# Kernel tuning notes

Hardware: AMD Instinct MI355X
Metric: run time of the kernel (lower is better)

## Reference

```python
import jax, jax.numpy as jnp
import numpy as np
from jax import lax

N = 100000   # n_nodes
E = 600000   # n_edges (no self loops by construction)
D = 128      # hidden_dim
L = 3        # n_hops
K = 5        # tail_k_threshold


def setup_inputs() -> dict:
    key = jax.random.key(0)
    ks = jax.random.split(key, 10)
    x = jax.random.normal(ks[0], (N, D), dtype=jnp.float32)
    src = jax.random.randint(ks[1], (E,), 0, N)
    off = jax.random.randint(ks[2], (E,), 1, N)
    dst = (src + off) % N  # guarantees dst != src (self loops removed in original)
    s = 1.0 / np.sqrt(D)
    def U(k, shape):
        return jax.random.uniform(k, shape, minval=-s, maxval=s, dtype=jnp.float32)
    return {
        "x": x,
        "G1": U(ks[3], (L, D, D)), "G2": U(ks[4], (L, D, D)),
        "B1": U(ks[5], (L, D, D)), "B2": U(ks[6], (L, D, D)),
        "R": U(ks[7], (L, D)),
        "edge_src": src, "edge_dst": dst,
    }


def _lrelu(v):
    return jax.nn.leaky_relu(v, 0.2)


def reference(x, G1, G2, B1, B2, R, edge_src, edge_dst):
    # row degrees of adj (A[src, dst] = 1)
    deg = jax.ops.segment_sum(jnp.ones(E, jnp.float32), edge_src, num_segments=N)
    inv_d = jnp.where(deg > 0, 1.0 / jnp.maximum(deg, 1.0), 0.0)   # left norm D^-1 A
    inv_d1 = 1.0 / (deg + 1.0)                                      # (A+I) left norm
    inv_d2 = 1.0 / (deg + 2.0)                                      # +1 virtual node
    w0, w1, w2 = inv_d[edge_src], inv_d1[edge_src], inv_d2[edge_src]
    head_mask = deg > K

    def spmm(w_edge, h):  # (D^-1 A) @ h via gather-scale-scatter
        return jax.ops.segment_sum(w_edge[:, None] * h[edge_dst], edge_src, num_segments=N)

    def propagate(head):
        h = x
        embs = [h]
        sups = []
        for l in range(L):
            nb = spmm(w0, h)
            ft = lax.stop_gradient(h)
            nbd = lax.stop_gradient(nb)
            gamma = _lrelu(ft @ G1[l].T + nbd @ G2[l].T) + 1.0
            beta = _lrelu(ft @ B1[l].T + nbd @ B2[l].T)
            m = ft + gamma * R[l] + beta - nbd   # missing_info (Relation, ablation=0)
            sups.append(m)
            if head:
                h = spmm(w1, h) + inv_d1[:, None] * h
            else:
                h = spmm(w2, h) + inv_d2[:, None] * h + m * inv_d2[:, None]
            embs.append(h)
        emb = jnp.mean(jnp.stack(embs, 0), 0)
        sup = jnp.mean(jnp.stack(sups, 0), 0)
        return emb, sup

    emb_h, _ = propagate(True)
    emb_t, _ = propagate(False)
    node_emb = jnp.where(head_mask[:, None], emb_h, emb_t)
    return node_emb
```

## Files before the change

### kernel.cpp

```cpp
#include <hip/hip_runtime.h>

#define N_NODES 100000
#define N_EDGES 600000
#define DIM 128
#define SCAN_B 1024
#define NCHUNK 98

typedef __attribute__((ext_vector_type(4))) float f32x4;
typedef __attribute__((ext_vector_type(8))) short bf16x8;
typedef __attribute__((ext_vector_type(4))) unsigned short u16x4;
typedef __attribute__((ext_vector_type(8))) unsigned short u16x8;

__device__ __forceinline__ unsigned short f2bf(float f) {
    union { float f; unsigned u; } cv; cv.f = f;
    unsigned r = (cv.u + 0x7FFFu + ((cv.u >> 16) & 1u)) >> 16;
    return (unsigned short)r;
}
__device__ __forceinline__ float bf2f(unsigned short v) {
    union { unsigned u; float f; } c; c.u = ((unsigned)v) << 16; return c.f;
}


__global__ void k_degree(const int* __restrict__ src, int* __restrict__ degi) {
    int e = blockIdx.x * 256 + threadIdx.x;
    if (e < N_EDGES) atomicAdd(&degi[src[e]], 1);
}

__global__ void k_chunksum(const int* __restrict__ degi, int* __restrict__ bsum) {
    __shared__ int sm[SCAN_B];
    int i = blockIdx.x * SCAN_B + threadIdx.x;
    sm[threadIdx.x] = (i < N_NODES) ? degi[i] : 0;
    __syncthreads();
    for (int s = SCAN_B / 2; s > 0; s >>= 1) {
        if (threadIdx.x < (unsigned)s) sm[threadIdx.x] += sm[threadIdx.x + s];
        __syncthreads();
    }
    if (threadIdx.x == 0) bsum[blockIdx.x] = sm[0];
}

__global__ void k_scanb(int* __restrict__ bsum, int nb) {
    __shared__ int sm[128];
    int t = threadIdx.x;
    int v = (t < nb) ? bsum[t] : 0;
    sm[t] = v; __syncthreads();
    for (int s = 1; s < 128; s <<= 1) {
        int a = (t >= s) ? sm[t - s] : 0;
        __syncthreads();
        sm[t] += a;
        __syncthreads();
    }
    if (t < nb) bsum[t] = sm[t] - v;
}

__global__ void k_rowptr(const int* __restrict__ degi, const int* __restrict__ bsum,
                         int* __restrict__ rowptr, int* __restrict__ cnt,
                         float* __restrict__ inv0, float* __restrict__ inv1,
                         float* __restrict__ inv2) {
    __shared__ int sm[SCAN_B];
    int i = blockIdx.x * SCAN_B + threadIdx.x;
    int v = (i < N_NODES) ? degi[i] : 0;
    sm[threadIdx.x] = v; __syncthreads();
    for (int s = 1; s < SCAN_B; s <<= 1) {
        int a = (threadIdx.x >= (unsigned)s) ? sm[threadIdx.x - s] : 0;
        __syncthreads();
        sm[threadIdx.x] += a;
        __syncthreads();
    }
    if (i < N_NODES) {
        int excl = bsum[blockIdx.x] + sm[threadIdx.x] - v;
        rowptr[i] = excl;
        cnt[i] = excl;
        float d = (float)v;
        inv0[i] = (v > 0) ? 1.0f / d : 0.0f;
        inv1[i] = 1.0f / (d + 1.0f);
        inv2[i] = 1.0f / (d + 2.0f);
    }
}

__global__ void k_fill(const int* __restrict__ src, const int* __restrict__ dst,
                       int* __restrict__ cnt, int* __restrict__ col) {
    int e = blockIdx.x * 256 + threadIdx.x;
    if (e < N_EDGES) {
        int pos = atomicAdd(&cnt[src[e]], 1);
        col[pos] = dst[e];
    }
}

__global__ void k_pack(const float* __restrict__ G1, const float* __restrict__ G2,
                       const float* __restrict__ B1, const float* __restrict__ B2,
                       short* __restrict__ Wp) {
    int idx = blockIdx.x * 256 + threadIdx.x;
    int j = idx & 7, lane = (idx >> 3) & 63, nt = (idx >> 9) & 15, kb = (idx >> 13) & 7, l = idx >> 16;
    int k = kb * 32 + (lane >> 4) * 8 + j;
    int n = nt * 16 + (lane & 15);
    float v;
    if (n < 128) {
        v = (k < 128) ? G1[(l * 128 + n) * 128 + k] : G2[(l * 128 + n) * 128 + (k - 128)];
    } else {
        int n2 = n - 128;
        v = (k < 128) ? B1[(l * 128 + n2) * 128 + k] : B2[(l * 128 + n2) * 128 + (k - 128)];
    }
    Wp[idx] = (short)f2bf(v);
}

__global__ void k_xcast(const float* __restrict__ x, unsigned short* __restrict__ xb) {
    int i = (blockIdx.x * 256 + threadIdx.x) * 4;
    f32x4 v = *(const f32x4*)(x + i);
    unsigned short o0 = f2bf(v[0]), o1 = f2bf(v[1]), o2 = f2bf(v[2]), o3 = f2bf(v[3]);
    unsigned long long pk = (unsigned long long)o0 | ((unsigned long long)o1 << 16)
                          | ((unsigned long long)o2 << 32) | ((unsigned long long)o3 << 48);
    *(unsigned long long*)(xb + i) = pk;
}


__device__ __forceinline__ void gather4(const u16x8* __restrict__ h8,
        const int* __restrict__ col, int start, int d, int lane, float* acc) {
    int c = lane & 15;
    int base = lane & 48;
    int dd = d < 16 ? d : 16;
    int idx = (c < dd) ? col[start + c] : 0;
    int dm = d;
    int tmx = __shfl_xor(dm, 16);
    dm = dm > tmx ? dm : tmx;
    tmx = __shfl_xor(dm, 32);
    dm = dm > tmx ? dm : tmx;
    int dmain = dm < 16 ? dm : 16;
    int e = 0;
    for (; e + 2 <= dmain; e += 2) {
        int c0 = __shfl(idx, base + e, 64);
        int c1 = __shfl(idx, base + e + 1, 64);
        if (e < d) {
            u16x8 v = h8[(size_t)c0 * 16 + c];
#pragma unroll
            for (int j = 0; j < 8; ++j) acc[j] += bf2f(v[j]);
        }
        if (e + 1 < d) {
            u16x8 v = h8[(size_t)c1 * 16 + c];
#pragma unroll
            for (int j = 0; j < 8; ++j) acc[j] += bf2f(v[j]);
        }
    }
    if (e < dmain) {
        int c0 = __shfl(idx, base + e, 64);
        if (e < d) {
            u16x8 v = h8[(size_t)c0 * 16 + c];
#pragma unroll
            for (int j = 0; j < 8; ++j) acc[j] += bf2f(v[j]);
        }
        ++e;
    }
    if (dm > 16) {
        for (; e < d; ++e) {
            int c0 = col[start + e];
            u16x8 v = h8[(size_t)c0 * 16 + c];
#pragma unroll
            for (int j = 0; j < 8; ++j) acc[j] += bf2f(v[j]);
        }
    }
}

__global__ __launch_bounds__(256) void k_agg_head4(
    const unsigned short* __restrict__ hsrc, unsigned short* __restrict__ hnext,
    const unsigned short* __restrict__ xb, const unsigned short* __restrict__ h1b,
    float* __restrict__ outp, const float* __restrict__ inv1,
    const int* __restrict__ rowptr, const int* __restrict__ degi,
    const int* __restrict__ col, int final_hop)
{
    int lane = threadIdx.x & 63;
    int wid = (blockIdx.x * 256 + threadIdx.x) >> 6;
    int g = lane >> 4, c = lane & 15;
    int row = wid * 4 + g;
    int start = rowptr[row], d = degi[row];
    float acc[8] = {0,0,0,0,0,0,0,0};
    gather4((const u16x8*)hsrc, col, start, d, lane, acc);
    u16x8 hv = ((const u16x8*)hsrc)[(size_t)row * 16 + c];
    float w = inv1[row];
    float hn[8];
#pragma unroll
    for (int j = 0; j < 8; ++j) hn[j] = w * (acc[j] + bf2f(hv[j]));
    if (!final_hop) {
        u16x8 ho;
#pragma unroll
        for (int j = 0; j < 8; ++j) ho[j] = f2bf(hn[j]);
        ((u16x8*)hnext)[(size_t)row * 16 + c] = ho;
    } else {
        u16x8 xv = ((const u16x8*)xb)[(size_t)row * 16 + c];
        u16x8 h1 = ((const u16x8*)h1b)[(size_t)row * 16 + c];
        f32x4 e0, e1;
#pragma unroll
        for (int j = 0; j < 4; ++j)
            e0[j] = 0.25f * (bf2f(xv[j]) + bf2f(h1[j]) + bf2f(hv[j]) + hn[j]);
#pragma unroll
        for (int j = 0; j < 4; ++j)
            e1[j] = 0.25f * (bf2f(xv[4 + j]) + bf2f(h1[4 + j]) + bf2f(hv[4 + j]) + hn[4 + j]);
        float* op = outp + (size_t)row * DIM + c * 8;
        *(f32x4*)op = e0;
        *(f32x4*)(op + 4) = e1;
    }
}

__global__ __launch_bounds__(256) void k_tail_fused(
    const unsigned short* __restrict__ hb,
    unsigned short* __restrict__ hA, int write_hA,
    unsigned short* __restrict__ hb_next,
    const unsigned short* __restrict__ xb, const unsigned short* __restrict__ h1b,
    float* __restrict__ outp,
    const float* __restrict__ Rl, const short* __restrict__ Wp,
    const float* __restrict__ inv0, const float* __restrict__ inv1,
    const float* __restrict__ inv2,
    const int* __restrict__ rowptr, const int* __restrict__ degi,
    const int* __restrict__ col, int last)
{
    __shared__ __align__(16) unsigned short sS[16][136];

    int wave = threadIdx.x >> 6, lane = threadIdx.x & 63;
    int rb = blockIdx.x * 16;

    {
        int g = lane >> 4, c = lane & 15;
        int row = rb + wave * 4 + g;
        int start = rowptr[row], d = degi[row];
        float acc[8] = {0,0,0,0,0,0,0,0};
        gather4((const u16x8*)hb, col, start, d, lane, acc);
        u16x8 so;
#pragma unroll
        for (int j = 0; j < 8; ++j) so[j] = f2bf(acc[j]);
        *(u16x8*)&sS[wave * 4 + g][c * 8] = so;
        if (write_hA) {
            u16x8 xv = ((const u16x8*)hb)[(size_t)row * 16 + c];
            float w1 = inv1[row];
            u16x8 ho;
#pragma unroll
            for (int j = 0; j < 8; ++j) ho[j] = f2bf(w1 * (acc[j] + bf2f(xv[j])));
            ((u16x8*)hA)[(size_t)row * 16 + c] = ho;
        }
    }
    __syncthreads();

    int q = lane >> 4, m = lane & 15;
    int rowA = rb + m;
    float w0 = inv0[rowA];
    const unsigned short* hrow = hb + (size_t)rowA * DIM + q * 8;
    const short* wl = Wp + lane * 8;

    const f32x4 vz = {0.f, 0.f, 0.f, 0.f};
    f32x4 aA[2] = {vz, vz}, aB[2] = {vz, vz};

#pragma unroll
    for (int kb = 0; kb < 4; ++kb) {
        bf16x8 ah = *(const bf16x8*)(hrow + kb * 32);
#pragma unroll
        for (int j = 0; j < 2; ++j) {
            bf16x8 b1v = *(const bf16x8*)(wl + (kb * 16 + 2 * wave + j) * 512);
            bf16x8 b2v = *(const bf16x8*)(wl + (kb * 16 + 2 * wave + 8 + j) * 512);
            aA[j] = __builtin_amdgcn_mfma_f32_16x16x32_bf16(ah, b1v, aA[j], 0, 0, 0);
            aB[j] = __builtin_amdgcn_mfma_f32_16x16x32_bf16(ah, b2v, aB[j], 0, 0, 0);
        }
    }
#pragma unroll
    for (int kb = 0; kb < 4; ++kb) {
        u16x8 sv = *(const u16x8*)&sS[m][kb * 32 + q * 8];
        bf16x8 as;
#pragma unroll
        for (int j = 0; j < 8; ++j) as[j] = (short)f2bf(w0 * bf2f(sv[j]));
#pragma unroll
        for (int j = 0; j < 2; ++j) {
            bf16x8 b1v = *(const bf16x8*)(wl + ((kb + 4) * 16 + 2 * wave + j) * 512);
            bf16x8 b2v = *(const bf16x8*)(wl + ((kb + 4) * 16 + 2 * wave + 8 + j) * 512);
            aA[j] = __builtin_amdgcn_mfma_f32_16x16x32_bf16(as, b1v, aA[j], 0, 0, 0);
            aB[j] = __builtin_amdgcn_mfma_f32_16x16x32_bf16(as, b2v, aB[j], 0, 0, 0);
        }
    }

    float Rv[2];
#pragma unroll
    for (int j = 0; j < 2; ++j) Rv[j] = Rl[(2 * wave + j) * 16 + m];

#pragma unroll
    for (int r = 0; r < 4; ++r) {
        int gi = rb + q * 4 + r;
        float wi0 = inv0[gi], wi2 = inv2[gi];
        int dgi = degi[gi];
#pragma unroll
        for (int j = 0; j < 2; ++j) {
            int cc = (2 * wave + j) * 16 + m;
            float z1 = aA[j][r], z2 = aB[j][r];
            float h = bf2f(hb[(size_t)gi * DIM + cc]);
            float sva = bf2f(sS[q * 4 + r][cc]);
            float ga = (z1 > 0.f ? z1 : 0.2f * z1) + 1.0f;
            float be = (z2 > 0.f ? z2 : 0.2f * z2);
            float mm = h + ga * Rv[j] + be - wi0 * sva;
            float hn = wi2 * (sva + h + mm);
            if (!last) {
                hb_next[(size_t)gi * DIM + cc] = f2bf(hn);
            } else if (dgi <= 5) {
                float xv = bf2f(xb[(size_t)gi * DIM + cc]);
                float t1 = bf2f(h1b[(size_t)gi * DIM + cc]);
                outp[(size_t)gi * DIM + cc] = 0.25f * (xv + t1 + h + hn);
            }
        }
    }
}


extern "C" void kernel_launch(void* const* d_in, const int* in_sizes, int n_in,
                              void* d_out, int out_size, void* d_ws, size_t ws_size,
                              hipStream_t stream) {
    const float* x  = (const float*)d_in[0];
    const float* G1 = (const float*)d_in[1];
    const float* G2 = (const float*)d_in[2];
    const float* B1 = (const float*)d_in[3];
    const float* B2 = (const float*)d_in[4];
    const float* R  = (const float*)d_in[5];
    const int* esrc = (const int*)d_in[6];
    const int* edst = (const int*)d_in[7];
    float* out = (float*)d_out;

    char* base = (char*)d_ws;
    size_t off = 0;
    auto alloc = [&](size_t b) -> void* {
        void* p = base + off;
        off = (off + b + 255) & ~(size_t)255;
        return p;
    };
    int* degi   = (int*)alloc(4 * N_NODES);
    int* rowptr = (int*)alloc(4 * N_NODES);
    int* cnt    = (int*)alloc(4 * N_NODES);
    int* bsum   = (int*)alloc(4 * 256);
    int* col    = (int*)alloc(4 * N_EDGES);
    float* inv0 = (float*)alloc(4 * N_NODES);
    float* inv1 = (float*)alloc(4 * N_NODES);
    float* inv2 = (float*)alloc(4 * N_NODES);
    short* Wp   = (short*)alloc(2 * 3 * 65536);
    unsigned short* xb = (unsigned short*)alloc(2ull * N_NODES * DIM);
    unsigned short* hA = (unsigned short*)alloc(2ull * N_NODES * DIM);
    unsigned short* hB = (unsigned short*)alloc(2ull * N_NODES * DIM);
    unsigned short* tA = (unsigned short*)alloc(2ull * N_NODES * DIM);
    unsigned short* tB = (unsigned short*)alloc(2ull * N_NODES * DIM);

    hipMemsetAsync(degi, 0, 4 * N_NODES, stream);
    k_degree<<<(N_EDGES + 255) / 256, 256, 0, stream>>>(esrc, degi);
    k_chunksum<<<NCHUNK, SCAN_B, 0, stream>>>(degi, bsum);
    k_scanb<<<1, 128, 0, stream>>>(bsum, NCHUNK);
    k_rowptr<<<NCHUNK, SCAN_B, 0, stream>>>(degi, bsum, rowptr, cnt, inv0, inv1, inv2);
    k_fill<<<(N_EDGES + 255) / 256, 256, 0, stream>>>(esrc, edst, cnt, col);
    k_pack<<<768, 256, 0, stream>>>(G1, G2, B1, B2, Wp);
    k_xcast<<<12500, 256, 0, stream>>>(x, xb);

    k_tail_fused<<<6250, 256, 0, stream>>>(xb, hA, 1, tA, xb, tA, out, R, Wp,
                                           inv0, inv1, inv2, rowptr, degi, col, 0);

    k_agg_head4<<<6250, 256, 0, stream>>>(hA, hB, xb, hA, out, inv1, rowptr, degi, col, 0);
    k_agg_head4<<<6250, 256, 0, stream>>>(hB, hB, xb, hA, out, inv1, rowptr, degi, col, 1);

    k_tail_fused<<<6250, 256, 0, stream>>>(tA, (unsigned short*)0, 0, tB, xb, tA, out,
                                           R + 128, Wp + 65536,
                                           inv0, inv1, inv2, rowptr, degi, col, 0);
    k_tail_fused<<<6250, 256, 0, stream>>>(tB, (unsigned short*)0, 0, tB, xb, tA, out,
                                           R + 256, Wp + 131072,
                                           inv0, inv1, inv2, rowptr, degi, col, 1);
}
```

Measured before the change: 480.6 us.

## Merge head and tail hop kernels into one launch and stage rows in LDS

Each hop's head-path aggregation and tail-path fused kernel now run in a single launch. Odd blocks do head rows and even blocks do tail rows, so the two independent streams overlap and there are fewer launches. The tail block loads its own h rows into shared memory once and reuses them for the MFMA A operand and the epilogue, instead of re-reading global memory. It also stages the next-hop output in LDS so each row goes out as one coalesced vector store. The final head pass writes the output only for head rows, avoiding writes the tail pass would overwrite. The cost is three LDS buffers per block, which may reduce occupancy, plus an extra barrier in the tail path.

New measurement: 523.6 us. +9.0%, slower.

```diff
diff --git a/kernel.cpp b/kernel.cpp
--- a/kernel.cpp
+++ b/kernel.cpp
@@ -159,51 +159,14 @@
     }
 }
 
-__global__ __launch_bounds__(256) void k_agg_head4(
-    const unsigned short* __restrict__ hsrc, unsigned short* __restrict__ hnext,
-    const unsigned short* __restrict__ xb, const unsigned short* __restrict__ h1b,
-    float* __restrict__ outp, const float* __restrict__ inv1,
-    const int* __restrict__ rowptr, const int* __restrict__ degi,
-    const int* __restrict__ col, int final_hop)
-{
-    int lane = threadIdx.x & 63;
-    int wid = (blockIdx.x * 256 + threadIdx.x) >> 6;
-    int g = lane >> 4, c = lane & 15;
-    int row = wid * 4 + g;
-    int start = rowptr[row], d = degi[row];
-    float acc[8] = {0,0,0,0,0,0,0,0};
-    gather4((const u16x8*)hsrc, col, start, d, lane, acc);
-    u16x8 hv = ((const u16x8*)hsrc)[(size_t)row * 16 + c];
-    float w = inv1[row];
-    float hn[8];
-#pragma unroll
-    for (int j = 0; j < 8; ++j) hn[j] = w * (acc[j] + bf2f(hv[j]));
-    if (!final_hop) {
-        u16x8 ho;
-#pragma unroll
-        for (int j = 0; j < 8; ++j) ho[j] = f2bf(hn[j]);
-        ((u16x8*)hnext)[(size_t)row * 16 + c] = ho;
-    } else {
-        u16x8 xv = ((const u16x8*)xb)[(size_t)row * 16 + c];
-        u16x8 h1 = ((const u16x8*)h1b)[(size_t)row * 16 + c];
-        f32x4 e0, e1;
-#pragma unroll
-        for (int j = 0; j < 4; ++j)
-            e0[j] = 0.25f * (bf2f(xv[j]) + bf2f(h1[j]) + bf2f(hv[j]) + hn[j]);
-#pragma unroll
-        for (int j = 0; j < 4; ++j)
-            e1[j] = 0.25f * (bf2f(xv[4 + j]) + bf2f(h1[4 + j]) + bf2f(hv[4 + j]) + hn[4 + j]);
-        float* op = outp + (size_t)row * DIM + c * 8;
-        *(f32x4*)op = e0;
-        *(f32x4*)(op + 4) = e1;
-    }
-}
-
-__global__ __launch_bounds__(256) void k_tail_fused(
+
+__device__ __forceinline__ void tail_block(
+    int rb,
+    unsigned short (*sH)[136], unsigned short (*sS)[136], unsigned short (*sO)[136],
     const unsigned short* __restrict__ hb,
     unsigned short* __restrict__ hA, int write_hA,
     unsigned short* __restrict__ hb_next,
-    const unsigned short* __restrict__ xb, const unsigned short* __restrict__ h1b,
+    const unsigned short* __restrict__ xb, const unsigned short* __restrict__ t1b,
     float* __restrict__ outp,
     const float* __restrict__ Rl, const short* __restrict__ Wp,
     const float* __restrict__ inv0, const float* __restrict__ inv1,
@@ -211,10 +174,7 @@
     const int* __restrict__ rowptr, const int* __restrict__ degi,
     const int* __restrict__ col, int last)
 {
-    __shared__ __align__(16) unsigned short sS[16][136];
-
     int wave = threadIdx.x >> 6, lane = threadIdx.x & 63;
-    int rb = blockIdx.x * 16;
 
     {
         int g = lane >> 4, c = lane & 15;
@@ -222,25 +182,24 @@
         int start = rowptr[row], d = degi[row];
         float acc[8] = {0,0,0,0,0,0,0,0};
         gather4((const u16x8*)hb, col, start, d, lane, acc);
+        u16x8 hv = ((const u16x8*)hb)[(size_t)row * 16 + c];
         u16x8 so;
 #pragma unroll
         for (int j = 0; j < 8; ++j) so[j] = f2bf(acc[j]);
         *(u16x8*)&sS[wave * 4 + g][c * 8] = so;
+        *(u16x8*)&sH[wave * 4 + g][c * 8] = hv;
         if (write_hA) {
-            u16x8 xv = ((const u16x8*)hb)[(size_t)row * 16 + c];
             float w1 = inv1[row];
             u16x8 ho;
 #pragma unroll
-            for (int j = 0; j < 8; ++j) ho[j] = f2bf(w1 * (acc[j] + bf2f(xv[j])));
+            for (int j = 0; j < 8; ++j) ho[j] = f2bf(w1 * (acc[j] + bf2f(hv[j])));
             ((u16x8*)hA)[(size_t)row * 16 + c] = ho;
         }
     }
     __syncthreads();
 
     int q = lane >> 4, m = lane & 15;
-    int rowA = rb + m;
-    float w0 = inv0[rowA];
-    const unsigned short* hrow = hb + (size_t)rowA * DIM + q * 8;
+    float w0 = inv0[rb + m];
     const short* wl = Wp + lane * 8;
 
     const f32x4 vz = {0.f, 0.f, 0.f, 0.f};
@@ -248,7 +207,7 @@
 
 #pragma unroll
     for (int kb = 0; kb < 4; ++kb) {
-        bf16x8 ah = *(const bf16x8*)(hrow + kb * 32);
+        bf16x8 ah = *(const bf16x8*)&sH[m][kb * 32 + q * 8];
 #pragma unroll
         for (int j = 0; j < 2; ++j) {
             bf16x8 b1v = *(const bf16x8*)(wl + (kb * 16 + 2 * wave + j) * 512);
@@ -285,20 +244,103 @@
         for (int j = 0; j < 2; ++j) {
             int cc = (2 * wave + j) * 16 + m;
             float z1 = aA[j][r], z2 = aB[j][r];
-            float h = bf2f(hb[(size_t)gi * DIM + cc]);
+            float h = bf2f(sH[q * 4 + r][cc]);
             float sva = bf2f(sS[q * 4 + r][cc]);
             float ga = (z1 > 0.f ? z1 : 0.2f * z1) + 1.0f;
             float be = (z2 > 0.f ? z2 : 0.2f * z2);
             float mm = h + ga * Rv[j] + be - wi0 * sva;
             float hn = wi2 * (sva + h + mm);
             if (!last) {
-                hb_next[(size_t)gi * DIM + cc] = f2bf(hn);
+                sO[q * 4 + r][cc] = f2bf(hn);
             } else if (dgi <= 5) {
                 float xv = bf2f(xb[(size_t)gi * DIM + cc]);
-                float t1 = bf2f(h1b[(size_t)gi * DIM + cc]);
+                float t1 = bf2f(t1b[(size_t)gi * DIM + cc]);
                 outp[(size_t)gi * DIM + cc] = 0.25f * (xv + t1 + h + hn);
             }
         }
+    }
+    if (!last) {
+        __syncthreads();
+        int g = lane >> 4, c = lane & 15;
+        int row = rb + wave * 4 + g;
+        ((u16x8*)hb_next)[(size_t)row * 16 + c] = *(u16x8*)&sO[wave * 4 + g][c * 8];
+    }
+}
+
+__device__ __forceinline__ void head_block(
+    int rb,
+    const unsigned short* __restrict__ hsrc, unsigned short* __restrict__ hnext,
+    const unsigned short* __restrict__ xb, const unsigned short* __restrict__ h1b,
+    float* __restrict__ outp, const float* __restrict__ inv1,
+    const int* __restrict__ rowptr, const int* __restrict__ degi,
+    const int* __restrict__ col, int final_hop)
+{
+    int wave = threadIdx.x >> 6, lane = threadIdx.x & 63;
+    int g = lane >> 4, c = lane & 15;
+    int row = rb + wave * 4 + g;
+    int start = rowptr[row], d = degi[row];
+    float acc[8] = {0,0,0,0,0,0,0,0};
+    gather4((const u16x8*)hsrc, col, start, d, lane, acc);
+    u16x8 hv = ((const u16x8*)hsrc)[(size_t)row * 16 + c];
+    float w = inv1[row];
+    float hn[8];
+#pragma unroll
+    for (int j = 0; j < 8; ++j) hn[j] = w * (acc[j] + bf2f(hv[j]));
+    if (!final_hop) {
+        u16x8 ho;
+#pragma unroll
+        for (int j = 0; j < 8; ++j) ho[j] = f2bf(hn[j]);
+        ((u16x8*)hnext)[(size_t)row * 16 + c] = ho;
+    } else if (d > 5) {
+        u16x8 xv = ((const u16x8*)xb)[(size_t)row * 16 + c];
+        u16x8 h1 = ((const u16x8*)h1b)[(size_t)row * 16 + c];
+        f32x4 e0, e1;
+#pragma unroll
+        for (int j = 0; j < 4; ++j)
+            e0[j] = 0.25f * (bf2f(xv[j]) + bf2f(h1[j]) + bf2f(hv[j]) + hn[j]);
+#pragma unroll
+        for (int j = 0; j < 4; ++j)
+            e1[j] = 0.25f * (bf2f(xv[4 + j]) + bf2f(h1[4 + j]) + bf2f(hv[4 + j]) + hn[4 + j]);
+        float* op = outp + (size_t)row * DIM + c * 8;
+        *(f32x4*)op = e0;
+        *(f32x4*)(op + 4) = e1;
+    }
+}
+
+
+__global__ __launch_bounds__(256) void k_fused0(
+    const unsigned short* __restrict__ xb, unsigned short* __restrict__ hA,
+    unsigned short* __restrict__ tA, float* __restrict__ outp,
+    const float* __restrict__ Rl, const short* __restrict__ Wp,
+    const float* __restrict__ inv0, const float* __restrict__ inv1,
+    const float* __restrict__ inv2,
+    const int* __restrict__ rowptr, const int* __restrict__ degi,
+    const int* __restrict__ col)
+{
+    __shared__ __align__(16) unsigned short sH[16][136], sS[16][136], sO[16][136];
+    tail_block(blockIdx.x * 16, sH, sS, sO, xb, hA, 1, tA, xb, tA, outp,
+               Rl, Wp, inv0, inv1, inv2, rowptr, degi, col, 0);
+}
+
+__global__ __launch_bounds__(256) void k_combined(
+    const unsigned short* __restrict__ tb, unsigned short* __restrict__ tb_next,
+    const unsigned short* __restrict__ hsrc, unsigned short* __restrict__ hnext,
+    const unsigned short* __restrict__ xb, const unsigned short* __restrict__ t1b,
+    const unsigned short* __restrict__ h1b, float* __restrict__ outp,
+    const float* __restrict__ Rl, const short* __restrict__ Wp,
+    const float* __restrict__ inv0, const float* __restrict__ inv1,
+    const float* __restrict__ inv2,
+    const int* __restrict__ rowptr, const int* __restrict__ degi,
+    const int* __restrict__ col, int lastfinal)
+{
+    __shared__ __align__(16) unsigned short sH[16][136], sS[16][136], sO[16][136];
+    int bid = blockIdx.x;
+    int rb = (bid >> 1) * 16;
+    if (bid & 1) {
+        head_block(rb, hsrc, hnext, xb, h1b, outp, inv1, rowptr, degi, col, lastfinal);
+    } else {
+        tail_block(rb, sH, sS, sO, tb, (unsigned short*)0, 0, tb_next, xb, t1b, outp,
+                   Rl, Wp, inv0, inv1, inv2, rowptr, degi, col, lastfinal);
     }
 }
 
@@ -347,16 +389,14 @@
     k_pack<<<768, 256, 0, stream>>>(G1, G2, B1, B2, Wp);
     k_xcast<<<12500, 256, 0, stream>>>(x, xb);
 
-    k_tail_fused<<<6250, 256, 0, stream>>>(xb, hA, 1, tA, xb, tA, out, R, Wp,
-                                           inv0, inv1, inv2, rowptr, degi, col, 0);
-
-    k_agg_head4<<<6250, 256, 0, stream>>>(hA, hB, xb, hA, out, inv1, rowptr, degi, col, 0);
-    k_agg_head4<<<6250, 256, 0, stream>>>(hB, hB, xb, hA, out, inv1, rowptr, degi, col, 1);
-
-    k_tail_fused<<<6250, 256, 0, stream>>>(tA, (unsigned short*)0, 0, tB, xb, tA, out,
-                                           R + 128, Wp + 65536,
-                                           inv0, inv1, inv2, rowptr, degi, col, 0);
-    k_tail_fused<<<6250, 256, 0, stream>>>(tB, (unsigned short*)0, 0, tB, xb, tA, out,
-                                           R + 256, Wp + 131072,
-                                           inv0, inv1, inv2, rowptr, degi, col, 1);
-}
+    k_fused0<<<6250, 256, 0, stream>>>(xb, hA, tA, out, R, Wp,
+                                       inv0, inv1, inv2, rowptr, degi, col);
+
+    k_combined<<<12500, 256, 0, stream>>>(tA, tB, hA, hB, xb, tA, hA, out,
+                                          R + 128, Wp + 65536,
+                                          inv0, inv1, inv2, rowptr, degi, col, 0);
+
+    k_combined<<<12500, 256, 0, stream>>>(tB, tB, hB, hB, xb, tA, hA, out,
+                                          R + 256, Wp + 131072,
+                                          inv0, inv1, inv2, rowptr, degi, col, 1);
+}
```
